# Optimization experiments

Hardware: AMD Instinct MI355X
Metric: run time of the kernel (lower is better)

Reference implementation:

```python
import jax, jax.numpy as jnp
import numpy as np

N, F, H, ES, EG, G, NC = 32768, 64, 4, 524288, 524288, 64, 10
BN_EPS = 1e-5


def setup_inputs():
    key = jax.random.key(0)
    ks = jax.random.split(key, 24)
    return {
        "x": jax.random.normal(ks[0], (N, F), jnp.float32),
        "edge_index": jax.random.randint(ks[1], (2, EG), 0, N),
        "batch": jnp.sort(jax.random.randint(ks[2], (N,), 0, G)),
        "scatter_idx": jax.random.randint(ks[3], (4, 2, ES), 0, N),
        "scatter_attr": jax.random.normal(ks[4], (4, ES), jnp.float32),
        "gat_W": jax.random.normal(ks[5], (4, F, H * F), jnp.float32) * 0.1,
        "gat_asrc": jax.random.normal(ks[6], (4, H, F), jnp.float32) * 0.1,
        "gat_adst": jax.random.normal(ks[7], (4, H, F), jnp.float32) * 0.1,
        "gat_b": jax.random.normal(ks[8], (4, H * F), jnp.float32) * 0.01,
        "mlp_W": jax.random.normal(ks[9], (4, H * F, F), jnp.float32) * 0.06,
        "mlp_b": jnp.zeros((4, F), jnp.float32),
        "mlp_g": jnp.ones((4, F), jnp.float32),
        "mlp_beta": jnp.zeros((4, F), jnp.float32),
        "fc1_W": jax.random.normal(ks[10], (F, 256), jnp.float32) * 0.1,
        "fc1_b": jnp.zeros((256,), jnp.float32),
        "fc1_g": jnp.ones((256,), jnp.float32),
        "fc1_beta": jnp.zeros((256,), jnp.float32),
        "fc2_W": jax.random.normal(ks[11], (256, 128), jnp.float32) * 0.06,
        "fc2_b": jnp.zeros((128,), jnp.float32),
        "fc2_g": jnp.ones((128,), jnp.float32),
        "fc2_beta": jnp.zeros((128,), jnp.float32),
        "fc3_W": jax.random.normal(ks[12], (128, NC), jnp.float32) * 0.08,
        "fc3_b": jnp.zeros((NC,), jnp.float32),
        "fc3_g": jnp.ones((NC,), jnp.float32),
        "fc3_beta": jnp.zeros((NC,), jnp.float32),
    }


def _solo_pass(idx, attr, x):
    # message: edge_attr * x[src]; aggregate: scatter-add at dst
    src, dst = idx[0], idx[1]
    return jax.ops.segment_sum(attr[:, None] * x[src], dst, num_segments=x.shape[0])


def _batchnorm(y, g, b):
    # training-mode BatchNorm1d: batch stats, biased variance
    mu = jnp.mean(y, axis=0)
    var = jnp.mean((y - mu) ** 2, axis=0)
    return (y - mu) * jax.lax.rsqrt(var + BN_EPS) * g + b


def _gat(x, W, asrc, adst, bias, src, dst):
    n = x.shape[0]
    h = (x @ W).reshape(n, H, F)                     # [N,H,F]
    a_s = jnp.sum(h * asrc, axis=-1)                 # [N,H]
    a_d = jnp.sum(h * adst, axis=-1)                 # [N,H]
    loop = jnp.arange(n)
    s2 = jnp.concatenate([src, loop])                # add self-loops (PyG default)
    d2 = jnp.concatenate([dst, loop])
    e = jax.nn.leaky_relu(a_s[s2] + a_d[d2], 0.2)    # [E2,H]
    m = jax.ops.segment_max(e, d2, num_segments=n)
    ex = jnp.exp(e - m[d2])
    denom = jax.ops.segment_sum(ex, d2, num_segments=n)
    alpha = ex / denom[d2]                           # softmax over in-edges of each dst
    out = jax.ops.segment_sum(alpha[:, :, None] * h[s2], d2, num_segments=n)
    return out.reshape(n, H * F) + bias              # concat heads + bias


def reference(x, edge_index, batch, scatter_idx, scatter_attr,
              gat_W, gat_asrc, gat_adst, gat_b, mlp_W, mlp_b, mlp_g, mlp_beta,
              fc1_W, fc1_b, fc1_g, fc1_beta, fc2_W, fc2_b, fc2_g, fc2_beta,
              fc3_W, fc3_b, fc3_g, fc3_beta):
    src, dst = edge_index[0], edge_index[1]
    x0 = _solo_pass(scatter_idx[0], scatter_attr[0], x)
    xh1 = jnp.abs(_solo_pass(scatter_idx[1], scatter_attr[1], x))
    xh2 = jnp.abs(_solo_pass(scatter_idx[2], scatter_attr[2], x))
    xh3 = jnp.abs(_solo_pass(scatter_idx[3], scatter_attr[3], x))
    x1 = _solo_pass(scatter_idx[0], scatter_attr[0], xh1)
    x2 = _solo_pass(scatter_idx[0], scatter_attr[0], xh2)
    x3 = _solo_pass(scatter_idx[0], scatter_attr[0], xh3)
    xs = [x0, x1, x2, x3]
    for i in range(4):
        g = _gat(xs[i], gat_W[i], gat_asrc[i], gat_adst[i], gat_b[i], src, dst)
        z = jax.nn.elu(g) @ mlp_W[i] + mlp_b[i]      # (dropout = identity in eval)
        xs[i] = _batchnorm(z, mlp_g[i], mlp_beta[i])
    x_stage1 = x + xs[0]
    x_stage2 = x_stage1 + xs[1] + xs[2] + xs[3]
    pooled = jax.ops.segment_sum(x_stage2, batch, num_segments=G)  # global_add_pool
    h1 = jax.nn.relu(_batchnorm(pooled @ fc1_W + fc1_b, fc1_g, fc1_beta))
    h2 = jax.nn.relu(_batchnorm(h1 @ fc2_W + fc2_b, fc2_g, fc2_beta))
    out = _batchnorm(h2 @ fc3_W + fc3_b, fc3_g, fc3_beta)
    return out
```

## Files before the change

### kernel.cpp

```cpp
#include <hip/hip_runtime.h>
#include <hip/hip_bf16.h>

#define N_NODES 32768
#define F_DIM 64
#define H_HEADS 4
#define HF 256
#define ES_EDGES 524288
#define EG_EDGES 524288
#define G_GRAPHS 64
#define NC_OUT 10
#define BN_EPS 1e-5f
#define NH (N_NODES * H_HEADS)
#define NF_ELEMS (N_NODES * F_DIM)
#define CAP 48
#define ESCAP 44
#define NBIN 64
#define BSTRIDE 8960

typedef short bf16x8 __attribute__((ext_vector_type(8)));
typedef float f32x4 __attribute__((ext_vector_type(4)));

__device__ __forceinline__ float eluf(float x) { return x > 0.f ? x : expm1f(x); }
__device__ __forceinline__ float lreluf(float x) { return x > 0.f ? x : 0.2f * x; }
__device__ __forceinline__ float bu2f(unsigned short v) {
    return __uint_as_float((unsigned)v << 16);
}
__device__ __forceinline__ unsigned short f2bu(float f) {
    union { __hip_bfloat16 b; unsigned short u; } cv;
    cv.b = __float2bfloat16(f);
    return cv.u;
}

struct P5i { const int* p[5]; };
struct P5f { const float* p[5]; };

__global__ __launch_bounds__(256) void k_binA_prep(
        P5i src, P5i dst, P5f attr, int* __restrict__ gcur,
        long long* __restrict__ staging,
        const float* __restrict__ gat_W, const float* __restrict__ mlp_W,
        unsigned short* __restrict__ gat_Wt, unsigned short* __restrict__ mlp_Wt,
        const float* __restrict__ x, unsigned short* __restrict__ xbf,
        const float* __restrict__ gat_asrc, const float* __restrict__ gat_adst,
        float* __restrict__ ws, float* __restrict__ wd) {
    int b = blockIdx.x;
    if (b < 2560) {
        __shared__ int hist[NBIN];
        __shared__ int base[NBIN];
        int g = b >> 9;
        int e0 = (b & 511) * 1024 + threadIdx.x;
        const int* dp = dst.p[g];
        const int* sp = src.p[g];
        const float* ap = attr.p[g];
        int d[4], s[4], bin[4];
        unsigned av[4];
#pragma unroll
        for (int k = 0; k < 4; ++k) {
            int e = e0 + k * 256;
            d[k] = dp[e]; s[k] = sp[e];
            av[k] = ap ? __float_as_uint(ap[e]) : 0u;
            bin[k] = d[k] >> 9;
        }
        if (threadIdx.x < NBIN) hist[threadIdx.x] = 0;
        __syncthreads();
#pragma unroll
        for (int k = 0; k < 4; ++k) atomicAdd(&hist[bin[k]], 1);
        __syncthreads();
        if (threadIdx.x < NBIN) {
            base[threadIdx.x] = atomicAdd(&gcur[g * NBIN + threadIdx.x],
                                          hist[threadIdx.x]);
            hist[threadIdx.x] = 0;
        }
        __syncthreads();
#pragma unroll
        for (int k = 0; k < 4; ++k) {
            int p = atomicAdd(&hist[bin[k]], 1);
            int pos = base[bin[k]] + p;
            if (pos < BSTRIDE) {
                long long rec = ((long long)av[k] << 32) |
                                (unsigned)(s[k] | ((d[k] & 0x1FF) << 15));
                staging[((size_t)g * NBIN + bin[k]) * BSTRIDE + pos] = rec;
            }
        }
    } else if (b < 3072) {
        int t = ((b - 2560) << 8) + threadIdx.x;
        if (t < 65536) {
            int layer = t >> 14, r = t & 16383;
            int n = r >> 6, k = r & 63;
            gat_Wt[t] = f2bu(gat_W[(size_t)layer * 16384 + k * 256 + n]);
        } else {
            int u = t - 65536;
            int layer = u >> 14, r = u & 16383;
            int n = r >> 8, k = r & 255;
            mlp_Wt[(size_t)layer * 16384 + r] =
                f2bu(mlp_W[(size_t)layer * 16384 + k * 64 + n]);
        }
    } else if (b < 5120) {
        int t = ((b - 3072) << 8) + threadIdx.x;
        float4 v = ((const float4*)x)[t];
        ushort4 o;
        o.x = f2bu(v.x); o.y = f2bu(v.y); o.z = f2bu(v.z); o.w = f2bu(v.w);
        ((ushort4*)xbf)[t] = o;
    } else {
        int q = b - 5120;
        int l = q >> 1, sel = q & 1;
        int h = threadIdx.x >> 6, k = threadIdx.x & 63;
        const float* Wl = gat_W + (size_t)l * 16384;
        const float* av = (sel ? gat_adst : gat_asrc) + l * 256 + h * 64;
        float s = 0.f;
#pragma unroll 8
        for (int f = 0; f < 64; ++f) s += Wl[k * 256 + h * 64 + f] * av[f];
        (sel ? wd : ws)[(l * 4 + h) * 64 + k] = s;
    }
}

__global__ __launch_bounds__(1024) void k_binB(
        const long long* __restrict__ staging, const int* __restrict__ gcur,
        int* __restrict__ cnt, int* __restrict__ bg0,
        long long* __restrict__ brecs) {
    __shared__ int lcnt[512];
    int g = blockIdx.x / NBIN;
    int bin = blockIdx.x % NBIN;
    if (threadIdx.x < 512) lcnt[threadIdx.x] = 0;
    __syncthreads();
    int cb = gcur[g * NBIN + bin];
    cb = cb < BSTRIDE ? cb : BSTRIDE;
    const long long* st = staging + ((size_t)g * NBIN + bin) * BSTRIDE;
    for (int idx = threadIdx.x; idx < cb; idx += 1024) {
        long long rec = st[idx];
        unsigned lo = (unsigned)rec;
        int s = lo & 0x7FFF;
        int dlow = (lo >> 15) & 0x1FF;
        int p = atomicAdd(&lcnt[dlow], 1);
        if (p >= CAP) continue;
        int d = (bin << 9) | dlow;
        if (g == 0) {
            bg0[d * CAP + p] = s;
        } else {
            long long r = (rec & 0xFFFFFFFF00000000ll) | (unsigned)s;
            brecs[((size_t)(g - 1) * N_NODES + d) * CAP + p] = r;
        }
    }
    __syncthreads();
    if (threadIdx.x < 512)
        cnt[g * N_NODES + (bin << 9) + threadIdx.x] = lcnt[threadIdx.x];
}

__global__ void k_sgather3(const ushort4* __restrict__ xb4, const int* __restrict__ cnt,
                           const int2* __restrict__ brecs, ushort4* __restrict__ xh4) {
    int g = blockIdx.y;
    int d = blockIdx.x * 4 + (threadIdx.x >> 6);
    int lane = threadIdx.x & 63;
    int chunk = lane & 15, quad = lane >> 4;
    int c = cnt[(g + 2) * N_NODES + d];
    c = c < CAP ? c : CAP;
    const int2* rec = brecs + ((size_t)(g + 1) * N_NODES + d) * CAP;
    float a0 = 0.f, a1 = 0.f, a2 = 0.f, a3 = 0.f;
    for (int j0 = 0; j0 < c; j0 += 4) {
        int j = j0 + quad;
        if (j < c) {
            int2 r = rec[j];
            float w = __int_as_float(r.y);
            ushort4 hv = xb4[(size_t)r.x * 16 + chunk];
            a0 += w * bu2f(hv.x); a1 += w * bu2f(hv.y);
            a2 += w * bu2f(hv.z); a3 += w * bu2f(hv.w);
        }
    }
    a0 += __shfl_xor(a0, 16); a0 += __shfl_xor(a0, 32);
    a1 += __shfl_xor(a1, 16); a1 += __shfl_xor(a1, 32);
    a2 += __shfl_xor(a2, 16); a2 += __shfl_xor(a2, 32);
    a3 += __shfl_xor(a3, 16); a3 += __shfl_xor(a3, 32);
    if (quad == 0) {
        ushort4 o;
        o.x = f2bu(a0); o.y = f2bu(a1); o.z = f2bu(a2); o.w = f2bu(a3);
        xh4[(size_t)g * (NF_ELEMS / 4) + d * 16 + chunk] = o;
    }
}

__global__ void k_sgather_quad(const ushort4* __restrict__ xb4,
                               const ushort4* __restrict__ xh4,
                               const int* __restrict__ cnt, const int2* __restrict__ brecs,
                               ushort4* __restrict__ xs4,
                               const float* __restrict__ wsg, const float* __restrict__ wdg,
                               float* __restrict__ a_s_all, float* __restrict__ a_d_all) {
    __shared__ float WS[1024], WD[1024];
    for (int i = threadIdx.x; i < 1024; i += 256) { WS[i] = wsg[i]; WD[i] = wdg[i]; }
    __syncthreads();
    int d = blockIdx.x * 4 + (threadIdx.x >> 6);
    int lane = threadIdx.x & 63;
    int chunk = lane & 15, quad = lane >> 4;
    int c = cnt[1 * N_NODES + d];
    c = c < CAP ? c : CAP;
    const int2* rec = brecs + (size_t)d * CAP;
    const ushort4* base = (quad == 0) ? xb4 : (xh4 + (size_t)(quad - 1) * (NF_ELEMS / 4));
    float a0 = 0.f, a1 = 0.f, a2 = 0.f, a3 = 0.f;
    int j = 0;
    for (; j + 2 <= c; j += 2) {
        int2 r0 = rec[j], r1 = rec[j + 1];
        float w0 = __int_as_float(r0.y), w1 = __int_as_float(r1.y);
        ushort4 h0 = base[(size_t)r0.x * 16 + chunk];
        ushort4 h1 = base[(size_t)r1.x * 16 + chunk];
        float v00 = bu2f(h0.x), v01 = bu2f(h0.y), v02 = bu2f(h0.z), v03 = bu2f(h0.w);
        float v10 = bu2f(h1.x), v11 = bu2f(h1.y), v12 = bu2f(h1.z), v13 = bu2f(h1.w);
        if (quad) {
            v00 = fabsf(v00); v01 = fabsf(v01); v02 = fabsf(v02); v03 = fabsf(v03);
            v10 = fabsf(v10); v11 = fabsf(v11); v12 = fabsf(v12); v13 = fabsf(v13);
        }
        a0 += w0 * v00 + w1 * v10; a1 += w0 * v01 + w1 * v11;
        a2 += w0 * v02 + w1 * v12; a3 += w0 * v03 + w1 * v13;
    }
    for (; j < c; ++j) {
        int2 r = rec[j];
        float w = __int_as_float(r.y);
        ushort4 h0 = base[(size_t)r.x * 16 + chunk];
        float v0 = bu2f(h0.x), v1 = bu2f(h0.y), v2 = bu2f(h0.z), v3 = bu2f(h0.w);
        if (quad) { v0 = fabsf(v0); v1 = fabsf(v1); v2 = fabsf(v2); v3 = fabsf(v3); }
        a0 += w * v0; a1 += w * v1; a2 += w * v2; a3 += w * v3;
    }
    const float* wsq = WS + quad * 256;
    const float* wdq = WD + quad * 256;
    float lsv[4], ldv[4];
#pragma unroll
    for (int h = 0; h < 4; ++h) {
        int o = h * 64 + chunk * 4;
        lsv[h] = a0 * wsq[o] + a1 * wsq[o + 1] + a2 * wsq[o + 2] + a3 * wsq[o + 3];
        ldv[h] = a0 * wdq[o] + a1 * wdq[o + 1] + a2 * wdq[o + 2] + a3 * wdq[o + 3];
    }
#pragma unroll
    for (int h = 0; h < 4; ++h) {
        lsv[h] += __shfl_xor(lsv[h], 1); lsv[h] += __shfl_xor(lsv[h], 2);
        lsv[h] += __shfl_xor(lsv[h], 4); lsv[h] += __shfl_xor(lsv[h], 8);
        ldv[h] += __shfl_xor(ldv[h], 1); ldv[h] += __shfl_xor(ldv[h], 2);
        ldv[h] += __shfl_xor(ldv[h], 4); ldv[h] += __shfl_xor(ldv[h], 8);
    }
    if (chunk == 0) {
        float4 vs; vs.x = lsv[0]; vs.y = lsv[1]; vs.z = lsv[2]; vs.w = lsv[3];
        ((float4*)a_s_all)[(size_t)quad * N_NODES + d] = vs;
        float4 vd; vd.x = ldv[0]; vd.y = ldv[1]; vd.z = ldv[2]; vd.w = ldv[3];
        ((float4*)a_d_all)[(size_t)quad * N_NODES + d] = vd;
    }
    ushort4 o;
    o.x = f2bu(a0); o.y = f2bu(a1); o.z = f2bu(a2); o.w = f2bu(a3);
    xs4[(size_t)quad * (NF_ELEMS / 4) + d * 16 + chunk] = o;
}

__global__ __launch_bounds__(256) void k_gat_mlp(
        const int* __restrict__ cnt, const int* __restrict__ bg0,
        const float* __restrict__ a_s_all, const float* __restrict__ a_d_all,
        const ushort4* __restrict__ xs4_all, const unsigned short* __restrict__ gWt,
        const float* __restrict__ gat_b,
        const unsigned short* __restrict__ mWt_all, const float* __restrict__ mlp_b,
        float* __restrict__ z4, float* __restrict__ sums_all,
        float* __restrict__ sumsq_all) {
    __shared__ unsigned short AG[16 * 264];
    __shared__ unsigned ESbuf[16 * ESCAP * 4];
    unsigned short* A2s = (unsigned short*)ESbuf;

    int lb = ((blockIdx.x & 7) << 10) | (blockIdx.x >> 3);
    int L = lb >> 11;
    int bx = lb & 2047;
    const float* a_sc = a_s_all + (size_t)L * N_NODES * 4;
    const float* a_dc = a_d_all + (size_t)L * N_NODES * 4;
    const ushort4* xs4 = xs4_all + (size_t)L * (NF_ELEMS / 4);
    const unsigned short* gWtL = gWt + (size_t)L * 16384;
    const float* gat_bL = gat_b + L * HF;
    const unsigned short* mWt = mWt_all + (size_t)L * 16384;
    const float* mbias = mlp_b + L * F_DIM;
    float* z = z4 + (size_t)L * NF_ELEMS;
    float* sums = sums_all + L * 64;
    float* sumsq = sumsq_all + L * 64;

    int wid = threadIdx.x >> 6, lane = threadIdx.x & 63;
    int dbase = bx * 16;
    int quad = lane >> 4;
    int e16 = lane & 15;
    for (int k = 0; k < 4; ++k) {
        int drow = wid * 4 + k;
        int d = dbase + drow;
        int c = cnt[d];
        c = c < CAP ? c : CAP;
        const int* col = bg0 + (size_t)d * CAP;
        float a_dd = a_dc[d * 4 + quad];
        float e_self = lreluf(a_sc[d * 4 + quad] + a_dd);
        float m = e_self;
        float ext[3]; int st[3];
#pragma unroll
        for (int t = 0; t < 3; ++t) {
            int j = t * 16 + e16;
            if (j < c) {
                int s = col[j];
                st[t] = s;
                float e = lreluf(a_sc[s * 4 + quad] + a_dd);
                ext[t] = e;
                m = fmaxf(m, e);
            } else { st[t] = 0; ext[t] = 0.f; }
        }
        m = fmaxf(m, __shfl_xor(m, 1)); m = fmaxf(m, __shfl_xor(m, 2));
        m = fmaxf(m, __shfl_xor(m, 4)); m = fmaxf(m, __shfl_xor(m, 8));
        float dsum = 0.f;
#pragma unroll
        for (int t = 0; t < 3; ++t) {
            float ex = (t * 16 + e16 < c) ? __expf(ext[t] - m) : 0.f;
            ext[t] = ex;
            dsum += ex;
        }
        dsum += __shfl_xor(dsum, 1); dsum += __shfl_xor(dsum, 2);
        dsum += __shfl_xor(dsum, 4); dsum += __shfl_xor(dsum, 8);
        float exs = __expf(e_self - m);
        float inv = 1.f / (dsum + exs);
#pragma unroll
        for (int t = 0; t < 3; ++t) {
            int j = t * 16 + e16;
            if (j < ESCAP)
                ESbuf[(drow * ESCAP + j) * 4 + quad] =
                    ((unsigned)f2bu(ext[t]) << 16) | (unsigned)(st[t] & 0xFFFF);
        }
        ushort4 sv = xs4[(size_t)d * 16 + e16];
        float ag0 = exs * bu2f(sv.x), ag1 = exs * bu2f(sv.y);
        float ag2 = exs * bu2f(sv.z), ag3 = exs * bu2f(sv.w);
        int cl = c < ESCAP ? c : ESCAP;
        int j = 0;
        for (; j + 4 <= cl; j += 4) {
            unsigned p0 = ESbuf[(drow * ESCAP + j    ) * 4 + quad];
            unsigned p1 = ESbuf[(drow * ESCAP + j + 1) * 4 + quad];
            unsigned p2 = ESbuf[(drow * ESCAP + j + 2) * 4 + quad];
            unsigned p3 = ESbuf[(drow * ESCAP + j + 3) * 4 + quad];
            ushort4 r0 = xs4[(size_t)(p0 & 0xFFFF) * 16 + e16];
            ushort4 r1 = xs4[(size_t)(p1 & 0xFFFF) * 16 + e16];
            ushort4 r2 = xs4[(size_t)(p2 & 0xFFFF) * 16 + e16];
            ushort4 r3 = xs4[(size_t)(p3 & 0xFFFF) * 16 + e16];
            float e0 = bu2f((unsigned short)(p0 >> 16));
            float e1 = bu2f((unsigned short)(p1 >> 16));
            float e2 = bu2f((unsigned short)(p2 >> 16));
            float e3 = bu2f((unsigned short)(p3 >> 16));
            ag0 += e0 * bu2f(r0.x) + e1 * bu2f(r1.x) + e2 * bu2f(r2.x) + e3 * bu2f(r3.x);
            ag1 += e0 * bu2f(r0.y) + e1 * bu2f(r1.y) + e2 * bu2f(r2.y) + e3 * bu2f(r3.y);
            ag2 += e0 * bu2f(r0.z) + e1 * bu2f(r1.z) + e2 * bu2f(r2.z) + e3 * bu2f(r3.z);
            ag3 += e0 * bu2f(r0.w) + e1 * bu2f(r1.w) + e2 * bu2f(r2.w) + e3 * bu2f(r3.w);
        }
        for (; j < cl; ++j) {
            unsigned p = ESbuf[(drow * ESCAP + j) * 4 + quad];
            ushort4 r = xs4[(size_t)(p & 0xFFFF) * 16 + e16];
            float e = bu2f((unsigned short)(p >> 16));
            ag0 += e * bu2f(r.x); ag1 += e * bu2f(r.y);
            ag2 += e * bu2f(r.z); ag3 += e * bu2f(r.w);
        }
        for (; j < c; ++j) {
            float e = __shfl(ext[2], (quad << 4) + (j - 32));
            int s = __shfl(st[2], j - 32);
            ushort4 r = xs4[(size_t)s * 16 + e16];
            ag0 += e * bu2f(r.x); ag1 += e * bu2f(r.y);
            ag2 += e * bu2f(r.z); ag3 += e * bu2f(r.w);
        }
        ushort4 o;
        o.x = f2bu(ag0 * inv); o.y = f2bu(ag1 * inv);
        o.z = f2bu(ag2 * inv); o.w = f2bu(ag3 * inv);
        *(ushort4*)(AG + drow * 264 + quad * 64 + e16 * 4) = o;
    }
    __syncthreads();
    {
        const unsigned short* agp = AG + e16 * 264 + wid * 64 + quad * 8;
        bf16x8 af0 = *(const bf16x8*)agp;
        bf16x8 af1 = *(const bf16x8*)(agp + 32);
#pragma unroll
        for (int nt = 0; nt < 4; ++nt) {
            int ng = wid * 64 + nt * 16 + e16;
            const unsigned short* bp = gWtL + (size_t)ng * 64 + quad * 8;
            bf16x8 b0 = *(const bf16x8*)bp;
            bf16x8 b1 = *(const bf16x8*)(bp + 32);
            f32x4 cc = {0.f, 0.f, 0.f, 0.f};
            cc = __builtin_amdgcn_mfma_f32_16x16x32_bf16(af0, b0, cc, 0, 0, 0);
            cc = __builtin_amdgcn_mfma_f32_16x16x32_bf16(af1, b1, cc, 0, 0, 0);
            float gb = gat_bL[ng];
#pragma unroll
            for (int r = 0; r < 4; ++r) {
                float v = eluf(cc[r] + gb);
                A2s[(quad * 4 + r) * 264 + ng] = f2bu(v);
            }
        }
    }
    __syncthreads();
    int n = lane & 15;
    f32x4 acc = {0.f, 0.f, 0.f, 0.f};
    const unsigned short* ap = A2s + n * 264 + quad * 8;
    const unsigned short* wtp = mWt + (size_t)(wid * 16 + n) * 256 + quad * 8;
#pragma unroll
    for (int ka = 0; ka < 8; ++ka) {
        bf16x8 af = *(const bf16x8*)(ap + ka * 32);
        bf16x8 bfr = *(const bf16x8*)(wtp + ka * 32);
        acc = __builtin_amdgcn_mfma_f32_16x16x32_bf16(af, bfr, acc, 0, 0, 0);
    }
    float b = mbias[wid * 16 + n];
    float s = 0.f, sq = 0.f;
#pragma unroll
    for (int r = 0; r < 4; ++r) {
        float v = acc[r] + b;
        z[(size_t)(dbase + quad * 4 + r) * 64 + wid * 16 + n] = v;
        s += v; sq += v * v;
    }
    s += __shfl_xor(s, 16); s += __shfl_xor(s, 32);
    sq += __shfl_xor(sq, 16); sq += __shfl_xor(sq, 32);
    if (quad == 0) {
        unsafeAtomicAdd(&sums[wid * 16 + n], s);
        unsafeAtomicAdd(&sumsq[wid * 16 + n], sq);
    }
}

__global__ void k_bnpool(const float* __restrict__ x, const float* __restrict__ z4,
                         const float* __restrict__ sums, const float* __restrict__ sumsq,
                         const float* __restrict__ g, const float* __restrict__ beta,
                         const int* __restrict__ batch, float* __restrict__ pooled) {
    int col = threadIdx.x & 63, rg = threadIdx.x >> 6;
    const float invN = 1.f / (float)N_NODES;
    float sc[4], off[4];
#pragma unroll
    for (int i = 0; i < 4; ++i) {
        float mu = sums[i * 64 + col] * invN;
        float var = sumsq[i * 64 + col] * invN - mu * mu;
        sc[i] = g[i * 64 + col] * rsqrtf(var + BN_EPS);
        off[i] = beta[i * 64 + col] - mu * sc[i];
    }
    float offt = off[0] + off[1] + off[2] + off[3];
    int r0 = blockIdx.x * 128 + rg * 32;
    int cur = -1;
    float acc = 0.f;
    for (int r = r0; r < r0 + 32; ++r) {
        int gb = batch[r];
        if (gb != cur) {
            if (cur >= 0) unsafeAtomicAdd(&pooled[cur * 64 + col], acc);
            cur = gb; acc = 0.f;
        }
        float v = x[(size_t)r * 64 + col] + offt;
#pragma unroll
        for (int i = 0; i < 4; ++i)
            v += sc[i] * z4[(size_t)i * NF_ELEMS + (size_t)r * 64 + col];
        acc += v;
    }
    if (cur >= 0) unsafeAtomicAdd(&pooled[cur * 64 + col], acc);
}

__global__ void k_h1(const float* __restrict__ pooled, const float* __restrict__ W1,
                     const float* __restrict__ b1, float* __restrict__ h1p) {
    int o = blockIdx.x * 256 + threadIdx.x;
    int m = o >> 8, n = o & 255;
    float s = b1[n];
#pragma unroll 8
    for (int k = 0; k < 64; ++k) s += pooled[m * 64 + k] * W1[k * 256 + n];
    h1p[o] = s;
}

__global__ __launch_bounds__(256) void k_h2(
        const float* __restrict__ h1p, const float* __restrict__ g1,
        const float* __restrict__ be1, const float* __restrict__ W2,
        const float* __restrict__ b2, float* __restrict__ h2p) {
    __shared__ float sT[256 * 65];
    __shared__ float sc[256], off[256];
    int t = threadIdx.x;
    for (int o = t; o < 16384; o += 256) {
        int m = o >> 8, k = o & 255;
        sT[k * 65 + m] = h1p[o];
    }
    __syncthreads();
    {
        int colc = t;
        float s = 0.f, sq = 0.f;
        for (int m = 0; m < 64; ++m) { float v = sT[colc * 65 + m]; s += v; sq += v * v; }
        float mu = s * (1.f / 64.f);
        float var = sq * (1.f / 64.f) - mu * mu;
        float scl = g1[colc] * rsqrtf(var + BN_EPS);
        sc[colc] = scl; off[colc] = be1[colc] - mu * scl;
    }
    __syncthreads();
    int m = t & 63, nl = t >> 6;
    int n = blockIdx.x * 4 + nl;
    float s = b2[n];
    for (int k = 0; k < 256; ++k) {
        float h = fmaxf(sT[k * 65 + m] * sc[k] + off[k], 0.f);
        s += h * W2[k * 128 + n];
    }
    h2p[m * 128 + n] = s;
}

__global__ __launch_bounds__(1024) void k_h3(
        const float* __restrict__ h2p, const float* __restrict__ g2,
        const float* __restrict__ be2, const float* __restrict__ W3,
        const float* __restrict__ b3, const float* __restrict__ g3,
        const float* __restrict__ be3, float* __restrict__ out) {
    __shared__ float sT[128 * 65];
    __shared__ float sc[128], off[128];
    __shared__ float h3[64 * NC_OUT];
    __shared__ float sc3[NC_OUT], off3[NC_OUT];
    int t = threadIdx.x;
    for (int o = t; o < 8192; o += 1024) {
        int m = o >> 7, k = o & 127;
        sT[k * 65 + m] = h2p[o];
    }
    __syncthreads();
    if (t < 128) {
        float s = 0.f, sq = 0.f;
        for (int m = 0; m < 64; ++m) { float v = sT[t * 65 + m]; s += v; sq += v * v; }
        float mu = s * (1.f / 64.f);
        float var = sq * (1.f / 64.f) - mu * mu;
        float scl = g2[t] * rsqrtf(var + BN_EPS);
        sc[t] = scl; off[t] = be2[t] - mu * scl;
    }
    __syncthreads();
    for (int o = t; o < 8192; o += 1024) {
        int m = o & 63, k = o >> 6;
        sT[k * 65 + m] = fmaxf(sT[k * 65 + m] * sc[k] + off[k], 0.f);
    }
    __syncthreads();
    if (t < 64 * NC_OUT) {
        int m = t / NC_OUT, n = t % NC_OUT;
        float s = b3[n];
        for (int k = 0; k < 128; ++k) s += sT[k * 65 + m] * W3[k * NC_OUT + n];
        h3[t] = s;
    }
    __syncthreads();
    if (t < NC_OUT) {
        float s = 0.f, sq = 0.f;
        for (int m = 0; m < 64; ++m) { float v = h3[m * NC_OUT + t]; s += v; sq += v * v; }
        float mu = s * (1.f / 64.f);
        float var = sq * (1.f / 64.f) - mu * mu;
        float scl = g3[t] * rsqrtf(var + BN_EPS);
        sc3[t] = scl; off3[t] = be3[t] - mu * scl;
    }
    __syncthreads();
    if (t < 64 * NC_OUT) out[t] = h3[t] * sc3[t % NC_OUT] + off3[t % NC_OUT];
}

extern "C" void kernel_launch(void* const* d_in, const int* in_sizes, int n_in,
                              void* d_out, int out_size, void* d_ws, size_t ws_size,
                              hipStream_t stream) {
    const float* x        = (const float*)d_in[0];
    const int*   ei       = (const int*)d_in[1];
    const int*   batch    = (const int*)d_in[2];
    const int*   sidx     = (const int*)d_in[3];
    const float* sattr    = (const float*)d_in[4];
    const float* gat_W    = (const float*)d_in[5];
    const float* gat_asrc = (const float*)d_in[6];
    const float* gat_adst = (const float*)d_in[7];
    const float* gat_b    = (const float*)d_in[8];
    const float* mlp_W    = (const float*)d_in[9];
    const float* mlp_b    = (const float*)d_in[10];
    const float* mlp_g    = (const float*)d_in[11];
    const float* mlp_beta = (const float*)d_in[12];
    const float* fc1_W    = (const float*)d_in[13];
    const float* fc1_b    = (const float*)d_in[14];
    const float* fc1_g    = (const float*)d_in[15];
    const float* fc1_beta = (const float*)d_in[16];
    const float* fc2_W    = (const float*)d_in[17];
    const float* fc2_b    = (const float*)d_in[18];
    const float* fc2_g    = (const float*)d_in[19];
    const float* fc2_beta = (const float*)d_in[20];
    const float* fc3_W    = (const float*)d_in[21];
    const float* fc3_b    = (const float*)d_in[22];
    const float* fc3_g    = (const float*)d_in[23];
    const float* fc3_beta = (const float*)d_in[24];

    char* wp = (char*)d_ws;
    auto alloc = [&](size_t bytes) {
        char* r = wp;
        wp += (bytes + 255) & ~(size_t)255;
        return (void*)r;
    };
    unsigned short* xs_bf = (unsigned short*)alloc(4 * (size_t)NF_ELEMS * 2);
    float* a_s_all = (float*)alloc(4 * (size_t)N_NODES * 4 * 4);
    float* a_d_all = (float*)alloc(4 * (size_t)N_NODES * 4 * 4);
    float* ws = (float*)alloc(1024 * 4);
    float* wd = (float*)alloc(1024 * 4);
    int*   cnt    = (int*)alloc(5 * N_NODES * 4);
    int*   gcur   = (int*)alloc(5 * NBIN * 4);
    float* sums   = (float*)alloc(4 * 64 * 4);
    float* sumsq  = (float*)alloc(4 * 64 * 4);
    float* pooled = (float*)alloc(G_GRAPHS * F_DIM * 4);
    const size_t ZBYTES = (5 * N_NODES + 5 * NBIN + 2 * 4 * 64 + G_GRAPHS * F_DIM) * 4;
    int*   bg0    = (int*)alloc((size_t)N_NODES * CAP * 4);
    unsigned short* gat_Wt = (unsigned short*)alloc(4 * 64 * 256 * 2);
    unsigned short* mlp_Wt = (unsigned short*)alloc(4 * 256 * 64 * 2);
    float* h1p = (float*)alloc(64 * 256 * 4);
    float* h2p = (float*)alloc(64 * 128 * 4);
    long long* staging = (long long*)alloc(5 * (size_t)NBIN * BSTRIDE * 8);
    char* U1 = (char*)alloc(4 * (size_t)NF_ELEMS * 2);
    unsigned short* xbf = (unsigned short*)U1;
    unsigned short* xh  = (unsigned short*)(U1 + (size_t)NF_ELEMS * 2);
    char* U2 = (char*)alloc(4 * (size_t)N_NODES * CAP * 8);
    long long* brecs = (long long*)U2;
    float* z4 = (float*)U2;

    P5i srcs, dsts; P5f attrs;
    srcs.p[0] = ei;              dsts.p[0] = ei + EG_EDGES;          attrs.p[0] = nullptr;
    for (int i = 0; i < 4; ++i) {
        srcs.p[i + 1]  = sidx + (size_t)i * 2 * ES_EDGES;
        dsts.p[i + 1]  = sidx + (size_t)i * 2 * ES_EDGES + ES_EDGES;
        attrs.p[i + 1] = sattr + (size_t)i * ES_EDGES;
    }

    hipMemsetAsync(cnt, 0, ZBYTES, stream);
    k_binA_prep<<<5128, 256, 0, stream>>>(srcs, dsts, attrs, gcur, staging,
                                          gat_W, mlp_W, gat_Wt, mlp_Wt, x, xbf,
                                          gat_asrc, gat_adst, ws, wd);

    k_binB<<<5 * NBIN, 1024, 0, stream>>>(staging, gcur, cnt, bg0, brecs);

    k_sgather3<<<dim3(N_NODES / 4, 3), 256, 0, stream>>>(
        (const ushort4*)xbf, cnt, (const int2*)brecs, (ushort4*)xh);
    k_sgather_quad<<<N_NODES / 4, 256, 0, stream>>>(
        (const ushort4*)xbf, (const ushort4*)xh, cnt, (const int2*)brecs,
        (ushort4*)xs_bf, ws, wd, a_s_all, a_d_all);

    k_gat_mlp<<<8192, 256, 0, stream>>>(
        cnt, bg0, a_s_all, a_d_all, (const ushort4*)xs_bf, gat_Wt, gat_b,
        mlp_Wt, mlp_b, z4, sums, sumsq);

    k_bnpool<<<256, 256, 0, stream>>>(x, z4, sums, sumsq, mlp_g, mlp_beta,
                                      batch, pooled);
    k_h1<<<64, 256, 0, stream>>>(pooled, fc1_W, fc1_b, h1p);
    k_h2<<<32, 256, 0, stream>>>(h1p, fc1_g, fc1_beta, fc2_W, fc2_b, h2p);
    k_h3<<<1, 1024, 0, stream>>>(h2p, fc2_g, fc2_beta, fc3_W, fc3_b,
                                 fc3_g, fc3_beta, (float*)d_out);
}
```

Baseline: 487.5 us.

## Restructure GAT aggregation so each lane owns a feature across all heads

The neighbor aggregation in the fused GAT+MLP kernel now assigns each lane one feature column and accumulates all four heads, instead of each lane owning four features of one head. Normalized fp32 attention weights and source indices are staged in separate shared arrays, the self-loop is folded in as an extra edge, and the packed bf16 weight/index encoding and the overflow shuffle path are dropped. Each gathered neighbor row is now read once per node rather than once per head. This cuts global gather traffic by about a factor of four, at the cost of 2-byte per-lane loads, more shared memory, and a changed AG padding stride.

New measurement: 487.6 us. About the same (+0.0%).

```diff
diff --git a/kernel.cpp b/kernel.cpp
--- a/kernel.cpp
+++ b/kernel.cpp
@@ -13,7 +13,6 @@
 #define NH (N_NODES * H_HEADS)
 #define NF_ELEMS (N_NODES * F_DIM)
 #define CAP 48
-#define ESCAP 44
 #define NBIN 64
 #define BSTRIDE 8960
 
@@ -251,9 +250,10 @@
         const unsigned short* __restrict__ mWt_all, const float* __restrict__ mlp_b,
         float* __restrict__ z4, float* __restrict__ sums_all,
         float* __restrict__ sumsq_all) {
-    __shared__ unsigned short AG[16 * 264];
-    __shared__ unsigned ESbuf[16 * ESCAP * 4];
-    unsigned short* A2s = (unsigned short*)ESbuf;
+    __shared__ float ESa[16 * 49 * 4];
+    __shared__ unsigned short EScol[16 * 50];
+    __shared__ unsigned short AG[16 * 268];
+    unsigned short* A2s = (unsigned short*)ESa;
 
     int lb = ((blockIdx.x & 7) << 10) | (blockIdx.x >> 3);
     int L = lb >> 11;
@@ -261,6 +261,7 @@
     const float* a_sc = a_s_all + (size_t)L * N_NODES * 4;
     const float* a_dc = a_d_all + (size_t)L * N_NODES * 4;
     const ushort4* xs4 = xs4_all + (size_t)L * (NF_ELEMS / 4);
+    const unsigned short* xsu = (const unsigned short*)xs4;
     const unsigned short* gWtL = gWt + (size_t)L * 16384;
     const float* gat_bL = gat_b + L * HF;
     const unsigned short* mWt = mWt_all + (size_t)L * 16384;
@@ -307,58 +308,50 @@
         dsum += __shfl_xor(dsum, 4); dsum += __shfl_xor(dsum, 8);
         float exs = __expf(e_self - m);
         float inv = 1.f / (dsum + exs);
+        float* ESrow = ESa + drow * 49 * 4;
+        unsigned short* ECrow = EScol + drow * 50;
 #pragma unroll
         for (int t = 0; t < 3; ++t) {
             int j = t * 16 + e16;
-            if (j < ESCAP)
-                ESbuf[(drow * ESCAP + j) * 4 + quad] =
-                    ((unsigned)f2bu(ext[t]) << 16) | (unsigned)(st[t] & 0xFFFF);
-        }
-        ushort4 sv = xs4[(size_t)d * 16 + e16];
-        float ag0 = exs * bu2f(sv.x), ag1 = exs * bu2f(sv.y);
-        float ag2 = exs * bu2f(sv.z), ag3 = exs * bu2f(sv.w);
-        int cl = c < ESCAP ? c : ESCAP;
+            if (j < c) {
+                ESrow[j * 4 + quad] = ext[t] * inv;
+                if (quad == 0) ECrow[j] = (unsigned short)st[t];
+            }
+        }
+        if (e16 == 0) ESrow[c * 4 + quad] = exs * inv;
+        if (lane == 0) ECrow[c] = (unsigned short)d;
+        int f = lane;
+        float ag0 = 0.f, ag1 = 0.f, ag2 = 0.f, ag3 = 0.f;
+        int cl = c + 1;
         int j = 0;
-        for (; j + 4 <= cl; j += 4) {
-            unsigned p0 = ESbuf[(drow * ESCAP + j    ) * 4 + quad];
-            unsigned p1 = ESbuf[(drow * ESCAP + j + 1) * 4 + quad];
-            unsigned p2 = ESbuf[(drow * ESCAP + j + 2) * 4 + quad];
-            unsigned p3 = ESbuf[(drow * ESCAP + j + 3) * 4 + quad];
-            ushort4 r0 = xs4[(size_t)(p0 & 0xFFFF) * 16 + e16];
-            ushort4 r1 = xs4[(size_t)(p1 & 0xFFFF) * 16 + e16];
-            ushort4 r2 = xs4[(size_t)(p2 & 0xFFFF) * 16 + e16];
-            ushort4 r3 = xs4[(size_t)(p3 & 0xFFFF) * 16 + e16];
-            float e0 = bu2f((unsigned short)(p0 >> 16));
-            float e1 = bu2f((unsigned short)(p1 >> 16));
-            float e2 = bu2f((unsigned short)(p2 >> 16));
-            float e3 = bu2f((unsigned short)(p3 >> 16));
-            ag0 += e0 * bu2f(r0.x) + e1 * bu2f(r1.x) + e2 * bu2f(r2.x) + e3 * bu2f(r3.x);
-            ag1 += e0 * bu2f(r0.y) + e1 * bu2f(r1.y) + e2 * bu2f(r2.y) + e3 * bu2f(r3.y);
-            ag2 += e0 * bu2f(r0.z) + e1 * bu2f(r1.z) + e2 * bu2f(r2.z) + e3 * bu2f(r3.z);
-            ag3 += e0 * bu2f(r0.w) + e1 * bu2f(r1.w) + e2 * bu2f(r2.w) + e3 * bu2f(r3.w);
-        }
-        for (; j < cl; ++j) {
-            unsigned p = ESbuf[(drow * ESCAP + j) * 4 + quad];
-            ushort4 r = xs4[(size_t)(p & 0xFFFF) * 16 + e16];
-            float e = bu2f((unsigned short)(p >> 16));
-            ag0 += e * bu2f(r.x); ag1 += e * bu2f(r.y);
-            ag2 += e * bu2f(r.z); ag3 += e * bu2f(r.w);
-        }
-        for (; j < c; ++j) {
-            float e = __shfl(ext[2], (quad << 4) + (j - 32));
-            int s = __shfl(st[2], j - 32);
-            ushort4 r = xs4[(size_t)s * 16 + e16];
-            ag0 += e * bu2f(r.x); ag1 += e * bu2f(r.y);
-            ag2 += e * bu2f(r.z); ag3 += e * bu2f(r.w);
-        }
-        ushort4 o;
-        o.x = f2bu(ag0 * inv); o.y = f2bu(ag1 * inv);
-        o.z = f2bu(ag2 * inv); o.w = f2bu(ag3 * inv);
-        *(ushort4*)(AG + drow * 264 + quad * 64 + e16 * 4) = o;
+        for (; j + 2 <= cl; j += 2) {
+            f32x4 al0 = *(const f32x4*)(ESrow + j * 4);
+            f32x4 al1 = *(const f32x4*)(ESrow + j * 4 + 4);
+            unsigned s0 = ECrow[j];
+            unsigned s1 = ECrow[j + 1];
+            float x0 = bu2f(xsu[s0 * 64u + (unsigned)f]);
+            float x1 = bu2f(xsu[s1 * 64u + (unsigned)f]);
+            ag0 += al0[0] * x0 + al1[0] * x1;
+            ag1 += al0[1] * x0 + al1[1] * x1;
+            ag2 += al0[2] * x0 + al1[2] * x1;
+            ag3 += al0[3] * x0 + al1[3] * x1;
+        }
+        if (j < cl) {
+            f32x4 al0 = *(const f32x4*)(ESrow + j * 4);
+            unsigned s0 = ECrow[j];
+            float x0 = bu2f(xsu[s0 * 64u + (unsigned)f]);
+            ag0 += al0[0] * x0; ag1 += al0[1] * x0;
+            ag2 += al0[2] * x0; ag3 += al0[3] * x0;
+        }
+        unsigned short* AGrow = AG + drow * 268;
+        AGrow[f]       = f2bu(ag0);
+        AGrow[64 + f]  = f2bu(ag1);
+        AGrow[128 + f] = f2bu(ag2);
+        AGrow[192 + f] = f2bu(ag3);
     }
     __syncthreads();
     {
-        const unsigned short* agp = AG + e16 * 264 + wid * 64 + quad * 8;
+        const unsigned short* agp = AG + e16 * 268 + wid * 64 + quad * 8;
         bf16x8 af0 = *(const bf16x8*)agp;
         bf16x8 af1 = *(const bf16x8*)(agp + 32);
 #pragma unroll
@@ -374,14 +367,14 @@
 #pragma unroll
             for (int r = 0; r < 4; ++r) {
                 float v = eluf(cc[r] + gb);
-                A2s[(quad * 4 + r) * 264 + ng] = f2bu(v);
+                A2s[(quad * 4 + r) * 268 + ng] = f2bu(v);
             }
         }
     }
     __syncthreads();
     int n = lane & 15;
     f32x4 acc = {0.f, 0.f, 0.f, 0.f};
-    const unsigned short* ap = A2s + n * 264 + quad * 8;
+    const unsigned short* ap = A2s + n * 268 + quad * 8;
     const unsigned short* wtp = mWt + (size_t)(wid * 16 + n) * 256 + quad * 8;
 #pragma unroll
     for (int ka = 0; ka < 8; ++ka) {
```
